# Kernel optimization log

Measured on AMD Instinct MI355X. Metric: run time of the kernel, lower is better.

## Reference

```python
import jax, jax.numpy as jnp
import numpy as np


def setup_inputs() -> dict:
    key = jax.random.key(0)
    ks = jax.random.split(key, 8)
    B, De, Do, T, H, W = 4, 128, 512, 4, 30, 52
    s = 0.05  # weight init scale
    return {
        "m_in": jax.random.normal(ks[0], (B, De, T, H, W), jnp.float32),
        "m_out": jax.random.normal(ks[1], (B, Do, T, H, W), jnp.float32),
        "q_in": jax.random.normal(ks[2], (B, De, H, W), jnp.float32),
        "q_out": jax.random.normal(ks[3], (B, Do, H, W), jnp.float32),
        "wr": jax.random.normal(ks[4], (Do, 2 * Do), jnp.float32) * s,
        "br": jnp.zeros((Do,), jnp.float32),
        "wu": jax.random.normal(ks[5], (Do, 2 * Do), jnp.float32) * s,
        "bu": jnp.zeros((Do,), jnp.float32),
        "wc": jax.random.normal(ks[6], (Do, 2 * Do), jnp.float32) * s,
        "bc": jnp.zeros((Do,), jnp.float32),
    }


def reference(m_in, m_out, q_in, q_out, wr, br, wu, bu, wc, bc):
    B, De, T, H, W = m_in.shape
    Do = m_out.shape[1]
    PROP_LAYERS = 5

    # --- memory read: pairwise frame attention (bmm + softmax + bmm) ---
    # keys: all T memory frames flattened; queries: current frame.
    mi = m_in.reshape(B, De, T * H * W)            # [B, De, THW]
    qi = q_in.reshape(B, De, H * W)                # [B, De, HW]
    p = jnp.einsum('bdk,bdq->bkq', mi, qi) / (De ** 0.5)  # [B, THW, HW]
    p = jax.nn.softmax(p, axis=1)                  # softmax over memory locations (dim=1 in torch)
    mem = jnp.einsum('bok,bkq->boq', m_out.reshape(B, Do, T * H * W), p)
    mem = mem.reshape(B, Do, H, W)                 # mem_mean; identical every propagate layer

    # --- ConvGRU_h (kernel_size=1 => per-pixel linear gates) ---
    def conv1x1(w, b, x):
        return jnp.einsum('oc,bchw->bohw', w, x) + b[None, :, None, None]

    def gru(x, h):
        xh = jnp.concatenate([x, h], axis=1)                       # [B, 2*Do, H, W]
        r = jax.nn.sigmoid(conv1x1(wr, br, xh))
        u = jax.nn.sigmoid(conv1x1(wu, bu, xh))
        c = jnp.tanh(conv1x1(wc, bc, jnp.concatenate([x, r * h], axis=1)))
        return h * (1.0 - u) + u * c

    q0 = q_out
    q = q_out
    for _ in range(PROP_LAYERS):
        q = gru(q, mem)  # original: q_out = ConvGRU_h(q_out, mem_mean)
    return jnp.concatenate([q, q0], axis=1)  # [B, 2*Do, H, W]
```

## Files before the change

kernel.cpp:

```cpp
#include <hip/hip_runtime.h>
#include <hip/hip_bf16.h>
#include <math.h>

typedef unsigned short u16;
typedef __attribute__((ext_vector_type(8))) short bf16x8;
typedef __attribute__((ext_vector_type(4))) float f32x4;

__device__ __forceinline__ u16 f2bf(float f) {
  union { float f; unsigned u; } x; x.f = f;
  unsigned r = x.u + 0x7fffu + ((x.u >> 16) & 1u);
  return (u16)(r >> 16);
}
__device__ __forceinline__ float bf2f(u16 h) {
  union { unsigned u; float f; } x; x.u = ((unsigned)h) << 16;
  return x.f;
}
__device__ __forceinline__ float sigmf(float x) {
  x = fminf(fmaxf(x, -30.f), 30.f);
  return 1.f / (1.f + __expf(-x));
}
__device__ __forceinline__ float tanh_fast(float x) {
  x = fminf(fmaxf(x, -15.f), 15.f);
  float t = __expf(2.f * x);
  return (t - 1.f) / (t + 1.f);
}

#define NB 4
#define DE 128
#define DO_ 512
#define HW 1560
#define THW 6240
#define NP 1664
#define KP 6272
#define PROP 5

#define BK 32

template<int MODE, int SPLIT, int BMT>
__global__ __launch_bounds__(256)
void gemm_bt(const u16* __restrict__ A, const u16* __restrict__ Bt,
             int K, int lda, int ldb, long a_bs, long b_bs,
             void* __restrict__ out0v, long o0_bs, int ld0,
             u16* __restrict__ out1, long o1_bs, int ld1,
             const void* __restrict__ e0v, long e0_bs,
             const void* __restrict__ e1v, long e1_bs,
             const void* __restrict__ e2v, long e2_bs,
             int nvalid, float scale)
{
  constexpr int WR = BMT / 64;
  constexpr int WC = 4 / WR;
  constexpr int NF = 8 / WC;
  constexpr int ASLOT = BMT * 4;
  constexpr int NISS = (ASLOT + 512) / 256;
  constexpr int RSH = (BMT == 128) ? 7 : 6;
  __shared__ u16 lds[(BMT + 128) * 32];

  const int tid = threadIdx.x;
  const int wave = tid >> 6, lane = tid & 63;
  const int kg = lane >> 4, lr = lane & 15;
  const int wrw = wave / WC, wcw = wave % WC;
  const int z = blockIdx.z;
  const long b = (SPLIT > 1) ? (z / SPLIT) : z;
  const int ks = K / SPLIT;
  const int k0 = (SPLIT > 1) ? (z % SPLIT) * ks : 0;
  const int m0 = blockIdx.x * BMT, n0 = blockIdx.y * 128;
  A += b * a_bs; Bt += b * b_bs;

  float* out0f = (float*)out0v;
  u16* out0h = (u16*)out0v;
  const float* e0f = (const float*)e0v;
  const u16* e0h = (const u16*)e0v;
  const u16* e1h = (const u16*)e1v;
  const u16* e2h = (const u16*)e2v;

  f32x4 acc[4][NF];
#pragma unroll
  for (int m = 0; m < 4; ++m)
#pragma unroll
    for (int n = 0; n < NF; ++n) acc[m][n] = (f32x4){0.f, 0.f, 0.f, 0.f};

  for (int kt = k0; kt < k0 + ks; kt += BK) {
#pragma unroll
    for (int i = 0; i < NISS; ++i) {
      int s = tid + 256 * i;
      const u16* src;
      if (s < ASLOT) {
        int row = s & (BMT - 1), g = s >> RSH;
        src = A + (long)(m0 + row) * lda + kt + g * 8;
      } else {
        int t = s - ASLOT;
        int row = t & 127, g = t >> 7;
        src = Bt + (long)(n0 + row) * ldb + kt + g * 8;
      }
      __builtin_amdgcn_global_load_lds(
          (const __attribute__((address_space(1))) void*)src,
          (__attribute__((address_space(3))) void*)&lds[(wave * 64 + 256 * i) * 8],
          16, 0, 0);
    }
    __syncthreads();
    bf16x8 af[4], bfr[NF];
#pragma unroll
    for (int m = 0; m < 4; ++m)
      af[m] = *(const bf16x8*)&lds[(kg * BMT + wrw * 64 + m * 16 + lr) * 8];
#pragma unroll
    for (int n = 0; n < NF; ++n)
      bfr[n] = *(const bf16x8*)&lds[(ASLOT + kg * 128 + (wcw * NF + n) * 16 + lr) * 8];
#pragma unroll
    for (int m = 0; m < 4; ++m)
#pragma unroll
      for (int n = 0; n < NF; ++n)
        acc[m][n] = __builtin_amdgcn_mfma_f32_16x16x32_bf16(af[m], bfr[n], acc[m][n], 0, 0, 0);
    __syncthreads();
  }

  if constexpr (MODE == 0) {
    float rs[4][4];
#pragma unroll
    for (int m = 0; m < 4; ++m)
#pragma unroll
      for (int j = 0; j < 4; ++j) rs[m][j] = 0.f;
#pragma unroll
    for (int m = 0; m < 4; ++m) {
      int rloc = wrw * 64 + m * 16 + kg * 4;
#pragma unroll
      for (int n = 0; n < NF; ++n) {
        int col = n0 + (wcw * NF + n) * 16 + lr;
#pragma unroll
        for (int j = 0; j < 4; ++j) {
          long row = m0 + rloc + j;
          float p = __expf(acc[m][n][j] * scale);
          bool valid = (col < nvalid);
          out1[b * o1_bs + row * ld1 + col] = valid ? f2bf(p) : (u16)0;
          rs[m][j] += valid ? p : 0.f;
        }
      }
    }
#pragma unroll
    for (int m = 0; m < 4; ++m)
#pragma unroll
      for (int j = 0; j < 4; ++j) {
#pragma unroll
        for (int msk = 1; msk < 16; msk <<= 1)
          rs[m][j] += __shfl_xor(rs[m][j], msk, 64);
      }
    float* zbuf = (float*)lds;
    if (lr == 0) {
#pragma unroll
      for (int m = 0; m < 4; ++m)
#pragma unroll
        for (int j = 0; j < 4; ++j)
          zbuf[wcw * 128 + wrw * 64 + m * 16 + kg * 4 + j] = rs[m][j];
    }
    __syncthreads();
    if (tid < 128)
      out0f[b * o0_bs + (long)blockIdx.y * NP + (m0 + tid)] = zbuf[tid] + zbuf[128 + tid];
    return;
  }

#pragma unroll
  for (int m = 0; m < 4; ++m) {
    int rloc = wrw * 64 + m * 16 + kg * 4;
#pragma unroll
    for (int n = 0; n < NF; ++n) {
      int col = n0 + (wcw * NF + n) * 16 + lr;
#pragma unroll
      for (int j = 0; j < 4; ++j) {
        long row = m0 + rloc + j;
        float v = acc[m][n][j];
        if constexpr (MODE == 5) {
          out0f[(long)z * o0_bs + row * ld0 + col] = v * e0f[b * e0_bs + row];
        } else if constexpr (MODE == 2) {
          out1[b * o1_bs + row * ld1 + col] = f2bf(v + e0f[col]);
        } else if constexpr (MODE == 3) {
          float gt = sigmf(v + bf2f(e0h[b * e0_bs + row * 1024 + col]));
          if (col < 512)
            out1[b * o1_bs + row * ld1 + 512 + col] =
                f2bf(gt * bf2f(e1h[b * e1_bs + row * 512 + col]));
          else
            out0h[b * o0_bs + row * ld0 + (col - 512)] = f2bf(gt);
        } else if constexpr (MODE == 4) {
          float cg = tanh_fast(v + e0f[col]);
          float u = bf2f(e1h[b * e1_bs + row * 512 + col]);
          float mm = bf2f(e2h[b * e2_bs + row * 512 + col]);
          float x = mm * (1.f - u) + u * cg;
          out1[b * o1_bs + row * ld1 + col] = f2bf(x);
          if (out0f) out0f[b * o0_bs + row * ld0 + col] = x;
        }
      }
    }
  }
}

__global__ void k_transpose_cast(const float* __restrict__ in, u16* __restrict__ out,
                                 int R, int C, int Cp, int out_ld,
                                 long in_bs, long out_bs) {
  __shared__ float t[32][33];
  long b = blockIdx.z;
  int c0 = blockIdx.x * 32, r0 = blockIdx.y * 32;
  int tx = threadIdx.x, ty = threadIdx.y;
#pragma unroll
  for (int i = 0; i < 32; i += 8) {
    int r = r0 + ty + i, c = c0 + tx;
    t[ty + i][tx] = (r < R && c < C) ? in[b * in_bs + (long)r * C + c] : 0.f;
  }
  __syncthreads();
#pragma unroll
  for (int i = 0; i < 32; i += 8) {
    int c = c0 + ty + i, r = r0 + tx;
    if (c < Cp && r < R)
      out[b * out_bs + (long)c * out_ld + r] = f2bf(t[tx][ty + i]);
  }
}

__global__ void k_cast_pad(const float* __restrict__ in, u16* __restrict__ out,
                           int Cin, int Cout, long in_bs, long out_bs) {
  int c = blockIdx.x * 256 + threadIdx.x;
  int r = blockIdx.y;
  long b = blockIdx.z;
  if (c >= Cout) return;
  out[b * out_bs + (long)r * Cout + c] =
      (c < Cin) ? f2bf(in[b * in_bs + (long)r * Cin + c]) : (u16)0;
}

__global__ void k_build_wru(const float* __restrict__ wr_, const float* __restrict__ wu_,
                            u16* __restrict__ wrux, u16* __restrict__ wruh) {
  int k = blockIdx.x * 256 + threadIdx.x;
  int m = blockIdx.y;
  if (k >= 512) return;
  const float* src = (m < 512) ? wr_ : wu_;
  int mm = m & 511;
  wrux[m * 512 + k] = f2bf(src[mm * 1024 + k]);
  wruh[m * 512 + k] = f2bf(src[mm * 1024 + 512 + k]);
}

__global__ void k_bias_ru(const float* __restrict__ br_, const float* __restrict__ bu_,
                          float* __restrict__ bias) {
  int i = blockIdx.x * 256 + threadIdx.x;
  if (i < 1024) bias[i] = (i < 512) ? br_[i] : bu_[i - 512];
}

__global__ void k_invz(const float* __restrict__ Zp, float* __restrict__ invZ) {
  int t = blockIdx.x * 256 + threadIdx.x;
  if (t >= NB * NP) return;
  int b = t / NP, q = t - b * NP;
  const float* base = Zp + (long)b * 49 * NP + q;
  float s = 0.f;
#pragma unroll
  for (int nb = 0; nb < 49; ++nb) s += base[(long)nb * NP];
  invZ[t] = 1.f / s;
}

__global__ void k_reduce_mem(const float* __restrict__ Ppart, u16* __restrict__ memTb) {
  long t = (long)blockIdx.x * 256 + threadIdx.x;
  const long bs = (long)NP * DO_;
  if (t >= (long)NB * bs / 4) return;
  long flat = t * 4;
  int b = (int)(flat / bs);
  long r = flat - (long)b * bs;
  f32x4 s = *(const f32x4*)&Ppart[(long)(b * 2) * bs + r] +
            *(const f32x4*)&Ppart[(long)(b * 2 + 1) * bs + r];
  uint2 pk;
  pk.x = (unsigned)f2bf(s[0]) | ((unsigned)f2bf(s[1]) << 16);
  pk.y = (unsigned)f2bf(s[2]) | ((unsigned)f2bf(s[3]) << 16);
  *(uint2*)&memTb[(long)b * bs + r] = pk;
}

__global__ void k_out_q(const float* __restrict__ Qfin, float* __restrict__ dout) {
  __shared__ float t[32][33];
  long b = blockIdx.z;
  int q0 = blockIdx.x * 32, ch0 = blockIdx.y * 32;
  int tx = threadIdx.x, ty = threadIdx.y;
#pragma unroll
  for (int i = 0; i < 32; i += 8)
    t[ty + i][tx] = Qfin[b * ((long)NP * 512) + (long)(q0 + ty + i) * 512 + ch0 + tx];
  __syncthreads();
#pragma unroll
  for (int i = 0; i < 32; i += 8) {
    int ch = ch0 + ty + i, q = q0 + tx;
    if (q < HW)
      dout[b * ((long)1024 * HW) + (long)ch * HW + q] = t[tx][ty + i];
  }
}

__global__ void k_copy_q0(const float4* __restrict__ src, float4* __restrict__ dst) {
  int idx = blockIdx.x * 256 + threadIdx.x;
  long b = blockIdx.z;
  const long n4 = (long)DO_ * HW / 4;
  if (idx < n4)
    dst[b * ((long)1024 * HW / 4) + n4 + idx] = src[b * n4 + idx];
}

extern "C" void kernel_launch(void* const* d_in, const int* in_sizes, int n_in,
                              void* d_out, int out_size, void* d_ws, size_t ws_size,
                              hipStream_t stream) {
  const float* m_in  = (const float*)d_in[0];
  const float* m_out = (const float*)d_in[1];
  const float* q_in  = (const float*)d_in[2];
  const float* q_out = (const float*)d_in[3];
  const float* wr    = (const float*)d_in[4];
  const float* br    = (const float*)d_in[5];
  const float* wu    = (const float*)d_in[6];
  const float* bu    = (const float*)d_in[7];
  const float* wc    = (const float*)d_in[8];
  const float* bc    = (const float*)d_in[9];
  float* dout = (float*)d_out;

  char* p = (char*)d_ws;
  size_t off = 0;
  auto alloc = [&](size_t bytes) { void* r = p + off; off += (bytes + 255) & ~(size_t)255; return r; };
  u16*   miT    = (u16*)alloc((size_t)NB * KP * DE * 2);
  u16*   qiT    = (u16*)alloc((size_t)NB * NP * DE * 2);
  u16*   Pt     = (u16*)alloc((size_t)NB * NP * KP * 2);
  float* invZ   = (float*)alloc((size_t)NB * NP * 4);
  u16*   moutb  = (u16*)alloc((size_t)NB * DO_ * KP * 2);
  u16*   memTb  = (u16*)alloc((size_t)NB * NP * DO_ * 2);
  u16*   chru   = (u16*)alloc((size_t)NB * NP * 1024 * 2);
  u16*   U      = (u16*)alloc((size_t)NB * NP * DO_ * 2);
  u16*   XRb    = (u16*)alloc((size_t)NB * NP * 1024 * 2);
  u16*   XRa    = (u16*)alloc((size_t)NB * NP * 1024 * 2);
  float* Qfin   = (float*)alloc((size_t)NB * NP * DO_ * 4);
  u16*   wrux   = (u16*)alloc((size_t)1024 * 512 * 2);
  u16*   wruh   = (u16*)alloc((size_t)1024 * 512 * 2);
  u16*   wcb    = (u16*)alloc((size_t)512 * 1024 * 2);
  float* biasru = (float*)alloc((size_t)1024 * 4);
  float* Ppart  = (float*)chru;
  float* Zp     = (float*)memTb;
  if (off > ws_size) return;

  k_build_wru<<<dim3(2, 1024), 256, 0, stream>>>(wr, wu, wrux, wruh);
  k_cast_pad<<<dim3(4, 512, 1), 256, 0, stream>>>(wc, wcb, 1024, 1024, 0, 0);
  k_bias_ru<<<dim3(4), 256, 0, stream>>>(br, bu, biasru);
  k_cast_pad<<<dim3(25, 512, NB), 256, 0, stream>>>(
      m_out, moutb, THW, KP, (long)DO_ * THW, (long)DO_ * KP);
  k_transpose_cast<<<dim3(196, 4, NB), dim3(32, 8), 0, stream>>>(
      m_in, miT, DE, THW, KP, DE, (long)DE * THW, (long)KP * DE);
  k_transpose_cast<<<dim3(52, 4, NB), dim3(32, 8), 0, stream>>>(
      q_in, qiT, DE, HW, NP, DE, (long)DE * HW, (long)NP * DE);
  k_transpose_cast<<<dim3(52, 16, NB), dim3(32, 8), 0, stream>>>(
      q_out, XRa, DO_, HW, NP, 1024, (long)DO_ * HW, (long)NP * 1024);

  gemm_bt<0, 1, 128><<<dim3(13, 49, NB), 256, 0, stream>>>(
      qiT, miT, DE, DE, DE, (long)NP * DE, (long)KP * DE,
      Zp, (long)49 * NP, 0, Pt, (long)NP * KP, KP,
      nullptr, 0, nullptr, 0, nullptr, 0, THW, 0.08838834764831845f);
  k_invz<<<dim3(26), 256, 0, stream>>>(Zp, invZ);

  gemm_bt<5, 2, 64><<<dim3(26, 4, NB * 2), 256, 0, stream>>>(
      Pt, moutb, KP, KP, KP, (long)NP * KP, (long)DO_ * KP,
      Ppart, (long)NP * DO_, DO_, nullptr, 0, 0,
      invZ, NP, nullptr, 0, nullptr, 0, 0, 0.f);
  k_reduce_mem<<<dim3(3328), 256, 0, stream>>>(Ppart, memTb);

  gemm_bt<2, 1, 64><<<dim3(26, 8, NB), 256, 0, stream>>>(
      memTb, wruh, DO_, DO_, DO_, (long)NP * DO_, 0,
      nullptr, 0, 0, chru, (long)NP * 1024, 1024,
      biasru, 0, nullptr, 0, nullptr, 0, 0, 0.f);

  u16* xr[2] = {XRa, XRb};
  for (int l = 0; l < PROP; ++l) {
    u16* cur = xr[l & 1];
    u16* nxt = xr[(l + 1) & 1];
    gemm_bt<3, 1, 64><<<dim3(26, 8, NB), 256, 0, stream>>>(
        cur, wrux, DO_, 1024, DO_, (long)NP * 1024, 0,
        U, (long)NP * DO_, DO_, cur, (long)NP * 1024, 1024,
        chru, (long)NP * 1024, memTb, (long)NP * DO_, nullptr, 0, 0, 0.f);
    gemm_bt<4, 1, 64><<<dim3(26, 4, NB), 256, 0, stream>>>(
        cur, wcb, 1024, 1024, 1024, (long)NP * 1024, 0,
        (l == PROP - 1) ? (void*)Qfin : nullptr, (long)NP * DO_, DO_,
        nxt, (long)NP * 1024, 1024,
        bc, 0, U, (long)NP * DO_, memTb, (long)NP * DO_, 0, 0.f);
  }

  k_out_q<<<dim3(49, 16, NB), dim3(32, 8), 0, stream>>>(Qfin, dout);
  k_copy_q0<<<dim3(780, 1, NB), 256, 0, stream>>>((const float4*)q_out, (float4*)dout);
}
```

Before: 736.7 us.

## Double-buffer GEMM LDS stages and add dedicated split-K P·V kernel with bf16 partials

The generic GEMM now double-buffers its LDS tiles, so the next K-slab is fetched while MFMAs run on the current one, and it takes a template K-tile size (64 for the GRU GEMMs). The P·V attention GEMM moves to a dedicated kernel that splits K four ways. It keeps each wave's full 128-column B fragment in registers, loaded straight from global and ping-ponged, and remaps blocks across XCDs. Partials are stored as bf16, and the softmax normaliser moves into the reduction kernel, which halves partial-sum traffic at some cost in precision.

```diff
diff --git a/kernel.cpp b/kernel.cpp
--- a/kernel.cpp
+++ b/kernel.cpp
@@ -34,9 +34,7 @@
 #define KP 6272
 #define PROP 5
 
-#define BK 32
-
-template<int MODE, int SPLIT, int BMT>
+template<int MODE, int BMT, int BKT>
 __global__ __launch_bounds__(256)
 void gemm_bt(const u16* __restrict__ A, const u16* __restrict__ Bt,
              int K, int lda, int ldb, long a_bs, long b_bs,
@@ -50,19 +48,18 @@
   constexpr int WR = BMT / 64;
   constexpr int WC = 4 / WR;
   constexpr int NF = 8 / WC;
-  constexpr int ASLOT = BMT * 4;
-  constexpr int NISS = (ASLOT + 512) / 256;
+  constexpr int KK = BKT / 32;
+  constexpr int ASLOT = BMT * BKT / 8;
+  constexpr int BSLOT = 128 * BKT / 8;
+  constexpr int NISS = (ASLOT + BSLOT) / 256;
   constexpr int RSH = (BMT == 128) ? 7 : 6;
-  __shared__ u16 lds[(BMT + 128) * 32];
+  __shared__ u16 lds[2][ASLOT + BSLOT][8];
 
   const int tid = threadIdx.x;
   const int wave = tid >> 6, lane = tid & 63;
   const int kg = lane >> 4, lr = lane & 15;
   const int wrw = wave / WC, wcw = wave % WC;
-  const int z = blockIdx.z;
-  const long b = (SPLIT > 1) ? (z / SPLIT) : z;
-  const int ks = K / SPLIT;
-  const int k0 = (SPLIT > 1) ? (z % SPLIT) * ks : 0;
+  const long b = blockIdx.z;
   const int m0 = blockIdx.x * BMT, n0 = blockIdx.y * 128;
   A += b * a_bs; Bt += b * b_bs;
 
@@ -73,13 +70,7 @@
   const u16* e1h = (const u16*)e1v;
   const u16* e2h = (const u16*)e2v;
 
-  f32x4 acc[4][NF];
-#pragma unroll
-  for (int m = 0; m < 4; ++m)
-#pragma unroll
-    for (int n = 0; n < NF; ++n) acc[m][n] = (f32x4){0.f, 0.f, 0.f, 0.f};
-
-  for (int kt = k0; kt < k0 + ks; kt += BK) {
+  auto stage = [&](int buf, int kt) {
 #pragma unroll
     for (int i = 0; i < NISS; ++i) {
       int s = tid + 256 * i;
@@ -88,28 +79,46 @@
         int row = s & (BMT - 1), g = s >> RSH;
         src = A + (long)(m0 + row) * lda + kt + g * 8;
       } else {
-        int t = s - ASLOT;
-        int row = t & 127, g = t >> 7;
+        int s2 = s - ASLOT;
+        int row = s2 & 127, g = s2 >> 7;
         src = Bt + (long)(n0 + row) * ldb + kt + g * 8;
       }
       __builtin_amdgcn_global_load_lds(
           (const __attribute__((address_space(1))) void*)src,
-          (__attribute__((address_space(3))) void*)&lds[(wave * 64 + 256 * i) * 8],
+          (__attribute__((address_space(3))) void*)&lds[buf][wave * 64 + 256 * i][0],
           16, 0, 0);
     }
-    __syncthreads();
-    bf16x8 af[4], bfr[NF];
-#pragma unroll
-    for (int m = 0; m < 4; ++m)
-      af[m] = *(const bf16x8*)&lds[(kg * BMT + wrw * 64 + m * 16 + lr) * 8];
-#pragma unroll
-    for (int n = 0; n < NF; ++n)
-      bfr[n] = *(const bf16x8*)&lds[(ASLOT + kg * 128 + (wcw * NF + n) * 16 + lr) * 8];
-#pragma unroll
-    for (int m = 0; m < 4; ++m)
+  };
+
+  f32x4 acc[4][NF];
+#pragma unroll
+  for (int m = 0; m < 4; ++m)
+#pragma unroll
+    for (int n = 0; n < NF; ++n) acc[m][n] = (f32x4){0.f, 0.f, 0.f, 0.f};
+
+  const int nt = K / BKT;
+  stage(0, 0);
+  __syncthreads();
+  for (int t = 0; t < nt; ++t) {
+    int cur = t & 1;
+    if (t + 1 < nt) stage(cur ^ 1, (t + 1) * BKT);
+    bf16x8 af[KK][4], bfr[KK][NF];
+#pragma unroll
+    for (int kk = 0; kk < KK; ++kk) {
+#pragma unroll
+      for (int m = 0; m < 4; ++m)
+        af[kk][m] = *(const bf16x8*)&lds[cur][(kk * 4 + kg) * BMT + wrw * 64 + m * 16 + lr][0];
 #pragma unroll
       for (int n = 0; n < NF; ++n)
-        acc[m][n] = __builtin_amdgcn_mfma_f32_16x16x32_bf16(af[m], bfr[n], acc[m][n], 0, 0, 0);
+        bfr[kk][n] = *(const bf16x8*)&lds[cur][ASLOT + (kk * 4 + kg) * 128 + (wcw * NF + n) * 16 + lr][0];
+    }
+#pragma unroll
+    for (int kk = 0; kk < KK; ++kk)
+#pragma unroll
+      for (int m = 0; m < 4; ++m)
+#pragma unroll
+        for (int n = 0; n < NF; ++n)
+          acc[m][n] = __builtin_amdgcn_mfma_f32_16x16x32_bf16(af[kk][m], bfr[kk][n], acc[m][n], 0, 0, 0);
     __syncthreads();
   }
 
@@ -167,9 +176,7 @@
       for (int j = 0; j < 4; ++j) {
         long row = m0 + rloc + j;
         float v = acc[m][n][j];
-        if constexpr (MODE == 5) {
-          out0f[(long)z * o0_bs + row * ld0 + col] = v * e0f[b * e0_bs + row];
-        } else if constexpr (MODE == 2) {
+        if constexpr (MODE == 2) {
           out1[b * o1_bs + row * ld1 + col] = f2bf(v + e0f[col]);
         } else if constexpr (MODE == 3) {
           float gt = sigmf(v + bf2f(e0h[b * e0_bs + row * 1024 + col]));
@@ -191,6 +198,92 @@
   }
 }
 
+__global__ __launch_bounds__(256, 2)
+void gemm_pv(const u16* __restrict__ Pt, const u16* __restrict__ moutb,
+             u16* __restrict__ Ppart)
+{
+  const int bid = blockIdx.x;
+  const int xcd = bid & 7, j = bid >> 3;
+  const int bz = 2 * xcd + (j >= 26);
+  const int mb = (j >= 26) ? (j - 26) : j;
+  const int b = bz >> 2, z = bz & 3;
+  const int m0 = mb * 64;
+  const int k0 = z * 1568;
+
+  const u16* A = Pt + (long)b * NP * KP;
+  const u16* B0;
+  {
+    const u16* Bb = moutb + (long)b * DO_ * KP;
+    B0 = Bb + (long)((threadIdx.x >> 6) * 128 + (threadIdx.x & 15)) * KP + ((threadIdx.x & 63) >> 4) * 8;
+  }
+
+  __shared__ u16 lds[2][2048];
+  const int tid = threadIdx.x;
+  const int wave = tid >> 6, lane = tid & 63;
+  const int kg = lane >> 4, lr = lane & 15;
+
+  auto stage = [&](int buf, int kt) {
+    int row = tid & 63, g = tid >> 6;
+    const u16* src = A + (long)(m0 + row) * KP + kt + g * 8;
+    __builtin_amdgcn_global_load_lds(
+        (const __attribute__((address_space(1))) void*)src,
+        (__attribute__((address_space(3))) void*)&lds[buf][(wave * 64) * 8],
+        16, 0, 0);
+  };
+
+  f32x4 acc[4][8];
+#pragma unroll
+  for (int m = 0; m < 4; ++m)
+#pragma unroll
+    for (int n = 0; n < 8; ++n) acc[m][n] = (f32x4){0.f, 0.f, 0.f, 0.f};
+
+  bf16x8 bra[8], brb[8];
+#pragma unroll
+  for (int n = 0; n < 8; ++n)
+    bra[n] = *(const bf16x8*)&B0[(long)n * 16 * KP + k0];
+  stage(0, k0);
+  __syncthreads();
+
+#define PV_STEP(BU, BL, T, CUR)                                                  \
+  {                                                                              \
+    if ((T) + 1 < 49) {                                                          \
+      int ktn = k0 + ((T) + 1) * 32;                                             \
+      _Pragma("unroll") for (int n = 0; n < 8; ++n)                              \
+          BL[n] = *(const bf16x8*)&B0[(long)n * 16 * KP + ktn];                  \
+      stage((CUR) ^ 1, ktn);                                                     \
+    }                                                                            \
+    bf16x8 af[4];                                                                \
+    _Pragma("unroll") for (int m = 0; m < 4; ++m)                                \
+        af[m] = *(const bf16x8*)&lds[CUR][(kg * 64 + m * 16 + lr) * 8];          \
+    _Pragma("unroll") for (int m = 0; m < 4; ++m)                                \
+        _Pragma("unroll") for (int n = 0; n < 8; ++n)                            \
+            acc[m][n] = __builtin_amdgcn_mfma_f32_16x16x32_bf16(af[m], BU[n],    \
+                                                                acc[m][n], 0, 0, 0); \
+    __syncthreads();                                                             \
+  }
+
+  for (int tp = 0; tp < 24; ++tp) {
+    PV_STEP(bra, brb, 2 * tp, 0);
+    PV_STEP(brb, bra, 2 * tp + 1, 1);
+  }
+  PV_STEP(bra, brb, 48, 0);
+#undef PV_STEP
+
+  u16* out = Ppart + (long)bz * NP * DO_;
+#pragma unroll
+  for (int m = 0; m < 4; ++m) {
+#pragma unroll
+    for (int n = 0; n < 8; ++n) {
+      int col = wave * 128 + n * 16 + lr;
+#pragma unroll
+      for (int j = 0; j < 4; ++j) {
+        int row = m0 + m * 16 + kg * 4 + j;
+        out[(long)row * DO_ + col] = f2bf(acc[m][n][j]);
+      }
+    }
+  }
+}
+
 __global__ void k_transpose_cast(const float* __restrict__ in, u16* __restrict__ out,
                                  int R, int C, int Cp, int out_ld,
                                  long in_bs, long out_bs) {
@@ -250,19 +343,33 @@
   invZ[t] = 1.f / s;
 }
 
-__global__ void k_reduce_mem(const float* __restrict__ Ppart, u16* __restrict__ memTb) {
+__global__ void k_reduce_mem(const u16* __restrict__ Ppart, const float* __restrict__ invZ,
+                             u16* __restrict__ memTb) {
   long t = (long)blockIdx.x * 256 + threadIdx.x;
   const long bs = (long)NP * DO_;
-  if (t >= (long)NB * bs / 4) return;
-  long flat = t * 4;
+  if (t >= (long)NB * bs / 8) return;
+  long flat = t * 8;
   int b = (int)(flat / bs);
   long r = flat - (long)b * bs;
-  f32x4 s = *(const f32x4*)&Ppart[(long)(b * 2) * bs + r] +
-            *(const f32x4*)&Ppart[(long)(b * 2 + 1) * bs + r];
-  uint2 pk;
-  pk.x = (unsigned)f2bf(s[0]) | ((unsigned)f2bf(s[1]) << 16);
-  pk.y = (unsigned)f2bf(s[2]) | ((unsigned)f2bf(s[3]) << 16);
-  *(uint2*)&memTb[(long)b * bs + r] = pk;
+  int q = (int)(r / DO_);
+  float s[8];
+#pragma unroll
+  for (int e = 0; e < 8; ++e) s[e] = 0.f;
+#pragma unroll
+  for (int z = 0; z < 4; ++z) {
+    uint4 v = *(const uint4*)&Ppart[(long)(b * 4 + z) * bs + r];
+    s[0] += bf2f((u16)(v.x & 0xffff)); s[1] += bf2f((u16)(v.x >> 16));
+    s[2] += bf2f((u16)(v.y & 0xffff)); s[3] += bf2f((u16)(v.y >> 16));
+    s[4] += bf2f((u16)(v.z & 0xffff)); s[5] += bf2f((u16)(v.z >> 16));
+    s[6] += bf2f((u16)(v.w & 0xffff)); s[7] += bf2f((u16)(v.w >> 16));
+  }
+  float iz = invZ[b * NP + q];
+  uint4 o;
+  o.x = (unsigned)f2bf(s[0] * iz) | ((unsigned)f2bf(s[1] * iz) << 16);
+  o.y = (unsigned)f2bf(s[2] * iz) | ((unsigned)f2bf(s[3] * iz) << 16);
+  o.z = (unsigned)f2bf(s[4] * iz) | ((unsigned)f2bf(s[5] * iz) << 16);
+  o.w = (unsigned)f2bf(s[6] * iz) | ((unsigned)f2bf(s[7] * iz) << 16);
+  *(uint4*)&memTb[(long)b * bs + r] = o;
 }
 
 __global__ void k_out_q(const float* __restrict__ Qfin, float* __restrict__ dout) {
@@ -323,7 +430,7 @@
   u16*   wruh   = (u16*)alloc((size_t)1024 * 512 * 2);
   u16*   wcb    = (u16*)alloc((size_t)512 * 1024 * 2);
   float* biasru = (float*)alloc((size_t)1024 * 4);
-  float* Ppart  = (float*)chru;
+  u16*   Ppart  = (u16*)chru;
   float* Zp     = (float*)memTb;
   if (off > ws_size) return;
 
@@ -339,19 +446,16 @@
   k_transpose_cast<<<dim3(52, 16, NB), dim3(32, 8), 0, stream>>>(
       q_out, XRa, DO_, HW, NP, 1024, (long)DO_ * HW, (long)NP * 1024);
 
-  gemm_bt<0, 1, 128><<<dim3(13, 49, NB), 256, 0, stream>>>(
+  gemm_bt<0, 128, 32><<<dim3(13, 49, NB), 256, 0, stream>>>(
       qiT, miT, DE, DE, DE, (long)NP * DE, (long)KP * DE,
       Zp, (long)49 * NP, 0, Pt, (long)NP * KP, KP,
       nullptr, 0, nullptr, 0, nullptr, 0, THW, 0.08838834764831845f);
   k_invz<<<dim3(26), 256, 0, stream>>>(Zp, invZ);
 
-  gemm_bt<5, 2, 64><<<dim3(26, 4, NB * 2), 256, 0, stream>>>(
-      Pt, moutb, KP, KP, KP, (long)NP * KP, (long)DO_ * KP,
-      Ppart, (long)NP * DO_, DO_, nullptr, 0, 0,
-      invZ, NP, nullptr, 0, nullptr, 0, 0, 0.f);
-  k_reduce_mem<<<dim3(3328), 256, 0, stream>>>(Ppart, memTb);
-
-  gemm_bt<2, 1, 64><<<dim3(26, 8, NB), 256, 0, stream>>>(
+  gemm_pv<<<dim3(416), 256, 0, stream>>>(Pt, moutb, Ppart);
+  k_reduce_mem<<<dim3(1664), 256, 0, stream>>>(Ppart, invZ, memTb);
+
+  gemm_bt<2, 64, 64><<<dim3(26, 8, NB), 256, 0, stream>>>(
       memTb, wruh, DO_, DO_, DO_, (long)NP * DO_, 0,
       nullptr, 0, 0, chru, (long)NP * 1024, 1024,
       biasru, 0, nullptr, 0, nullptr, 0, 0, 0.f);
@@ -360,11 +464,11 @@
   for (int l = 0; l < PROP; ++l) {
     u16* cur = xr[l & 1];
     u16* nxt = xr[(l + 1) & 1];
-    gemm_bt<3, 1, 64><<<dim3(26, 8, NB), 256, 0, stream>>>(
+    gemm_bt<3, 64, 64><<<dim3(26, 8, NB), 256, 0, stream>>>(
         cur, wrux, DO_, 1024, DO_, (long)NP * 1024, 0,
         U, (long)NP * DO_, DO_, cur, (long)NP * 1024, 1024,
         chru, (long)NP * 1024, memTb, (long)NP * DO_, nullptr, 0, 0, 0.f);
-    gemm_bt<4, 1, 64><<<dim3(26, 4, NB), 256, 0, stream>>>(
+    gemm_bt<4, 64, 64><<<dim3(26, 4, NB), 256, 0, stream>>>(
         cur, wcb, 1024, 1024, 1024, (long)NP * 1024, 0,
         (l == PROP - 1) ? (void*)Qfin : nullptr, (long)NP * DO_, DO_,
         nxt, (long)NP * 1024, 1024,
```

New measurement: 679.1 us. 1.08x faster.
